# Performance work log

Hardware: AMD Instinct MI355X
Metric: run time of the kernel (lower is better)

The kernel has to match this reference:

```python
import jax, jax.numpy as jnp
import numpy as np

E, H, HD = 2048, 32, 64
SCALE = HD ** -0.5


def setup_inputs() -> dict:
    key = jax.random.key(0)
    ks = jax.random.split(key, 11)
    B, T, P = 16, 4, 4096
    S = P + T
    return {
        "hidden_states": jax.random.normal(ks[0], (B, T, E), jnp.float32),
        "past_key": jax.random.normal(ks[1], (1, H, P, HD), jnp.float32),
        "past_value": jax.random.normal(ks[2], (1, H, P, HD), jnp.float32),
        "attention_mask": jnp.zeros((B, 1, T, S), jnp.float32),
        "Wq": jax.random.normal(ks[3], (E, E), jnp.float32) * 0.02,
        "bq": jax.random.normal(ks[4], (E,), jnp.float32) * 0.02,
        "Wk": jax.random.normal(ks[5], (E, E), jnp.float32) * 0.02,
        "bk": jax.random.normal(ks[6], (E,), jnp.float32) * 0.02,
        "Wv": jax.random.normal(ks[7], (E, E), jnp.float32) * 0.02,
        "bv": jax.random.normal(ks[8], (E,), jnp.float32) * 0.02,
        "Wo": jax.random.normal(ks[9], (E, E), jnp.float32) * 0.02,
        "bo": jax.random.normal(ks[10], (E,), jnp.float32) * 0.02,
    }


def _shape(x, B, S):
    # [B,S,E] -> [B,H,S,hd]
    return x.reshape(B, S, H, HD).transpose(0, 2, 1, 3)


def reference(hidden_states, past_key, past_value, attention_mask,
              Wq, bq, Wk, bk, Wv, bv, Wo, bo):
    B, T, _ = hidden_states.shape
    # projections (torch Linear: x @ W.T + b); query pre-scaled
    q = _shape(hidden_states @ Wq.T + bq, B, T) * SCALE   # [B,H,T,hd]
    k_new = _shape(hidden_states @ Wk.T + bk, B, T)       # [B,H,T,hd]
    v_new = _shape(hidden_states @ Wv.T + bv, B, T)
    # cache stored with batch 1, broadcast (torch repeat) to B, then concat
    k_past = jnp.broadcast_to(past_key, (B,) + past_key.shape[1:])
    v_past = jnp.broadcast_to(past_value, (B,) + past_value.shape[1:])
    k = jnp.concatenate([k_past, k_new], axis=2)          # [B,H,S,hd]
    v = jnp.concatenate([v_past, v_new], axis=2)
    scores = jnp.einsum('bhtd,bhsd->bhts', q, k)          # [B,H,T,S]
    scores = scores + attention_mask                      # mask is [B,1,T,S]
    scores = jnp.maximum(scores, jnp.finfo(scores.dtype).min)
    w = jax.nn.softmax(scores, axis=-1)
    out = jnp.einsum('bhts,bhsd->bhtd', w, v)             # [B,H,T,hd]
    out = out.transpose(0, 2, 1, 3).reshape(B, T, E)
    return out @ Wo.T + bo
```

## Files before the change

### kernel.cpp

```cpp
#include <hip/hip_runtime.h>
#include <hip/hip_bf16.h>


typedef float f4 __attribute__((ext_vector_type(4)));
typedef short s8v __attribute__((ext_vector_type(8)));

#define NEG_HUGE (-3.402823466e38f)

__device__ inline unsigned short f2bs(float x) {
  union { float f; unsigned int u; } a; a.f = x;
  unsigned int u = a.u;
  u += 0x7fffu + ((u >> 16) & 1u);
  return (unsigned short)(u >> 16);
}
__device__ inline float bs2f(unsigned short s) {
  union { unsigned int u; float f; } a; a.u = ((unsigned int)s) << 16;
  return a.f;
}
__device__ inline unsigned int pk2(float a, float b) {
  union { __hip_bfloat162 v; unsigned int u; } c;
  c.v = __float22bfloat162_rn(make_float2(a, b));
  return c.u;
}
__device__ inline unsigned long long pack4(float a, float b, float c, float d) {
  return (unsigned long long)pk2(a, b) | ((unsigned long long)pk2(c, d) << 32);
}
__device__ inline s8v cvt8(f4 a, f4 b) {
  union { s8v s; unsigned int u[4]; } r;
  r.u[0] = pk2(a[0], a[1]); r.u[1] = pk2(a[2], a[3]);
  r.u[2] = pk2(b[0], b[1]); r.u[3] = pk2(b[2], b[3]);
  return r.s;
}
__device__ inline f4 mfma16(s8v a, s8v b, f4 c) {
  return __builtin_amdgcn_mfma_f32_16x16x32_bf16(a, b, c, 0, 0, 0);
}
__device__ inline f4 fzero() { f4 z = {0.f,0.f,0.f,0.f}; return z; }
__device__ inline float wave_sum(float v) {
  #pragma unroll
  for (int off = 32; off; off >>= 1) v += __shfl_xor(v, off, 64);
  return v;
}

__global__ __launch_bounds__(256) void k_qkv(
    const float* __restrict__ hs, const float* __restrict__ Wq,
    const float* __restrict__ Wk, const float* __restrict__ Wv,
    float* __restrict__ part) {
  __shared__ __align__(16) unsigned short As[64 * 264];
  const int n0 = blockIdx.x * 64;
  const int k0 = blockIdx.y * 256;
  const int p = n0 >> 11;
  const int c0 = n0 & 2047;
  const float* W = (p == 0) ? Wq : (p == 1) ? Wk : Wv;
  const int t = threadIdx.x, lane = t & 63, w = t >> 6;
  const int cl = lane & 15, quad = lane >> 4;

  #pragma unroll
  for (int i = 0; i < 16; ++i) {
    int idx4 = t + (i << 8);
    int row = idx4 >> 6;
    int col = (idx4 & 63) << 2;
    f4 v = *reinterpret_cast<const f4*>(hs + row * 2048 + k0 + col);
    *reinterpret_cast<unsigned long long*>(&As[row * 264 + col]) =
        pack4(v[0], v[1], v[2], v[3]);
  }
  __syncthreads();

  f4 acc[4];
  #pragma unroll
  for (int i = 0; i < 4; ++i) acc[i] = fzero();

  const int cw = c0 + w * 16 + cl;
  const float* wbase = W + (size_t)cw * 2048 + k0;
  #pragma unroll
  for (int ks2 = 0; ks2 < 8; ++ks2) {
    const int kb = ks2 * 32 + quad * 8;
    f4 w0 = *reinterpret_cast<const f4*>(wbase + kb);
    f4 w1 = *reinterpret_cast<const f4*>(wbase + kb + 4);
    s8v bf = cvt8(w0, w1);
    #pragma unroll
    for (int mt = 0; mt < 4; ++mt) {
      s8v af = *reinterpret_cast<const s8v*>(&As[(mt * 16 + cl) * 264 + kb]);
      acc[mt] = mfma16(af, bf, acc[mt]);
    }
  }
  float* outp = part + (size_t)blockIdx.y * 64 * 6144;
  #pragma unroll
  for (int mt = 0; mt < 4; ++mt)
    #pragma unroll
    for (int rg = 0; rg < 4; ++rg) {
      int r = mt * 16 + quad * 4 + rg;
      outp[r * 6144 + n0 + w * 16 + cl] = acc[mt][rg];
    }
}

__global__ __launch_bounds__(256) void k_qkv_red(
    const float* __restrict__ part, const float* __restrict__ bq,
    const float* __restrict__ bk, const float* __restrict__ bv,
    unsigned short* __restrict__ qws, float* __restrict__ knew,
    float* __restrict__ vnew) {
  const int i4 = blockIdx.x * 256 + threadIdx.x;
  const int base = i4 * 4;
  const int r = base / 6144;
  const int n = base - r * 6144;
  f4 s = *reinterpret_cast<const f4*>(part + base);
  #pragma unroll
  for (int ks = 1; ks < 8; ++ks) {
    f4 p2 = *reinterpret_cast<const f4*>(part + (size_t)ks * 393216 + base);
    #pragma unroll
    for (int j = 0; j < 4; ++j) s[j] += p2[j];
  }
  const int p = n >> 11, c = n & 2047;
  const int h = c >> 6, d = c & 63;
  const int b = r >> 2, tt = r & 3;
  if (p == 0) {
    f4 bb = *reinterpret_cast<const f4*>(bq + c);
    uint2 pw;
    pw.x = pk2((s[0] + bb[0]) * 0.125f, (s[1] + bb[1]) * 0.125f);
    pw.y = pk2((s[2] + bb[2]) * 0.125f, (s[3] + bb[3]) * 0.125f);
    *reinterpret_cast<uint2*>(qws + h * 4608 + r * 72 + d) = pw;
  } else if (p == 1) {
    f4 bb = *reinterpret_cast<const f4*>(bk + c);
    f4 o;
    #pragma unroll
    for (int j = 0; j < 4; ++j) o[j] = s[j] + bb[j];
    *reinterpret_cast<f4*>(knew + ((h * 16 + b) * 4 + tt) * 64 + d) = o;
  } else {
    f4 bb = *reinterpret_cast<const f4*>(bv + c);
    f4 o;
    #pragma unroll
    for (int j = 0; j < 4; ++j) o[j] = s[j] + bb[j];
    *reinterpret_cast<f4*>(vnew + ((h * 16 + b) * 4 + tt) * 64 + d) = o;
  }
}

__global__ __launch_bounds__(256) void k_flash(
    const unsigned short* __restrict__ qws, const float* __restrict__ Kp,
    const float* __restrict__ Vp, const float* __restrict__ mask,
    float* __restrict__ Opart, float* __restrict__ mpart,
    float* __restrict__ lpart) {
  __shared__ __align__(16) unsigned short Pl[64 * 264];
  __shared__ float redm[4 * 64];
  __shared__ float reds[4 * 64];
  const int bx = blockIdx.x;
  const int h = bx & 31, cch = bx >> 5;
  const int s0 = cch * 256;
  const int t = threadIdx.x, lane = t & 63, w = t >> 6;
  const int cl = lane & 15, quad = lane >> 4;
  const float* Kh = Kp + (size_t)h * 4096 * 64;
  const float* Vh = Vp + (size_t)h * 4096 * 64;

  s8v qf[4][2];
  #pragma unroll
  for (int qt = 0; qt < 4; ++qt)
    #pragma unroll
    for (int k2 = 0; k2 < 2; ++k2)
      qf[qt][k2] = *reinterpret_cast<const s8v*>(
          qws + h * 4608 + (qt * 16 + cl) * 72 + k2 * 32 + quad * 8);

  f4 acc[4][4];
  #pragma unroll
  for (int si = 0; si < 4; ++si)
    #pragma unroll
    for (int qt = 0; qt < 4; ++qt) acc[si][qt] = fzero();

  #pragma unroll
  for (int si = 0; si < 4; ++si) {
    const float* kr = Kh + (size_t)(s0 + w * 64 + si * 16 + cl) * 64 + quad * 8;
    #pragma unroll
    for (int k2 = 0; k2 < 2; ++k2) {
      f4 k0v = *reinterpret_cast<const f4*>(kr + k2 * 32);
      f4 k1v = *reinterpret_cast<const f4*>(kr + k2 * 32 + 4);
      s8v ak = cvt8(k0v, k1v);
      #pragma unroll
      for (int qt = 0; qt < 4; ++qt)
        acc[si][qt] = mfma16(ak, qf[qt][k2], acc[si][qt]);
    }
  }

  #pragma unroll
  for (int si = 0; si < 4; ++si)
    #pragma unroll
    for (int qt = 0; qt < 4; ++qt) {
      f4 mv = *reinterpret_cast<const f4*>(
          mask + (size_t)(qt * 16 + cl) * 4100 + s0 + w * 64 + si * 16 + quad * 4);
      #pragma unroll
      for (int rg = 0; rg < 4; ++rg)
        acc[si][qt][rg] = fmaxf(acc[si][qt][rg] + mv[rg], NEG_HUGE);
    }

  #pragma unroll
  for (int qt = 0; qt < 4; ++qt) {
    float m = NEG_HUGE;
    #pragma unroll
    for (int si = 0; si < 4; ++si)
      #pragma unroll
      for (int rg = 0; rg < 4; ++rg) m = fmaxf(m, acc[si][qt][rg]);
    m = fmaxf(m, __shfl_xor(m, 16, 64));
    m = fmaxf(m, __shfl_xor(m, 32, 64));
    if (quad == 0) redm[w * 64 + qt * 16 + cl] = m;
  }
  __syncthreads();

  float mq[4];
  #pragma unroll
  for (int qt = 0; qt < 4; ++qt) {
    int q = qt * 16 + cl;
    mq[qt] = fmaxf(fmaxf(redm[q], redm[64 + q]),
                   fmaxf(redm[128 + q], redm[192 + q]));
    if (w == 0 && quad == 0) mpart[(h * 16 + cch) * 64 + q] = mq[qt];
  }
  #pragma unroll
  for (int qt = 0; qt < 4; ++qt) {
    float sum = 0.f;
    #pragma unroll
    for (int si = 0; si < 4; ++si) {
      f4 e;
      #pragma unroll
      for (int rg = 0; rg < 4; ++rg) {
        e[rg] = __expf(acc[si][qt][rg] - mq[qt]);
        sum += e[rg];
      }
      uint2 pw;
      pw.x = pk2(e[0], e[1]);
      pw.y = pk2(e[2], e[3]);
      *reinterpret_cast<uint2*>(
          &Pl[(qt * 16 + cl) * 264 + w * 64 + si * 16 + quad * 4]) = pw;
    }
    sum += __shfl_xor(sum, 16, 64);
    sum += __shfl_xor(sum, 32, 64);
    if (quad == 0) reds[w * 64 + qt * 16 + cl] = sum;
  }
  __syncthreads();

  if (w == 0 && quad == 0) {
    #pragma unroll
    for (int qt = 0; qt < 4; ++qt) {
      int q = qt * 16 + cl;
      lpart[(h * 16 + cch) * 64 + q] =
          reds[q] + reds[64 + q] + reds[128 + q] + reds[192 + q];
    }
  }

  f4 oacc[4];
  #pragma unroll
  for (int mt = 0; mt < 4; ++mt) oacc[mt] = fzero();
  const int dcol = w * 16 + cl;
  #pragma unroll
  for (int k2 = 0; k2 < 8; ++k2) {
    const int sb = k2 * 32 + quad * 8;
    const float* vb = Vh + (size_t)(s0 + sb) * 64 + dcol;
    f4 v0, v1;
    v0[0] = vb[0];   v0[1] = vb[64];  v0[2] = vb[128]; v0[3] = vb[192];
    v1[0] = vb[256]; v1[1] = vb[320]; v1[2] = vb[384]; v1[3] = vb[448];
    s8v bvv = cvt8(v0, v1);
    #pragma unroll
    for (int mt = 0; mt < 4; ++mt) {
      s8v pa = *reinterpret_cast<const s8v*>(&Pl[(mt * 16 + cl) * 264 + sb]);
      oacc[mt] = mfma16(pa, bvv, oacc[mt]);
    }
  }
  float* ob = Opart + (size_t)(h * 16 + cch) * 64 * 64;
  #pragma unroll
  for (int mt = 0; mt < 4; ++mt)
    #pragma unroll
    for (int rg = 0; rg < 4; ++rg)
      ob[(mt * 16 + quad * 4 + rg) * 64 + dcol] = oacc[mt][rg];
}

__global__ __launch_bounds__(256) void k_merge(
    const unsigned short* __restrict__ qws, const float* __restrict__ knew,
    const float* __restrict__ vnew, const float* __restrict__ mask,
    const float* __restrict__ Opart, const float* __restrict__ mpart,
    const float* __restrict__ lpart, unsigned short* __restrict__ attn) {
  const int bx = blockIdx.x;
  const int h = bx & 31, b = bx >> 5;
  const int tt = threadIdx.x >> 6;
  const int d = threadIdx.x & 63;
  const int r = b * 4 + tt;
  float qd = bs2f(qws[h * 4608 + r * 72 + d]);
  float scn[4];
  #pragma unroll
  for (int tp = 0; tp < 4; ++tp) {
    float kn = knew[((h * 16 + b) * 4 + tp) * 64 + d];
    float s = wave_sum(qd * kn);
    s += mask[(size_t)r * 4100 + 4096 + tp];
    scn[tp] = fmaxf(s, NEG_HUGE);
  }
  float mi[16], li[16];
  float mtot = NEG_HUGE;
  #pragma unroll
  for (int i = 0; i < 16; ++i) {
    mi[i] = mpart[(h * 16 + i) * 64 + r];
    li[i] = lpart[(h * 16 + i) * 64 + r];
    mtot = fmaxf(mtot, mi[i]);
  }
  #pragma unroll
  for (int tp = 0; tp < 4; ++tp) mtot = fmaxf(mtot, scn[tp]);
  float ltot = 0.f, od = 0.f;
  #pragma unroll
  for (int i = 0; i < 16; ++i) {
    float fct = __expf(mi[i] - mtot);
    ltot += li[i] * fct;
    od += Opart[((size_t)(h * 16 + i) * 64 + r) * 64 + d] * fct;
  }
  #pragma unroll
  for (int tp = 0; tp < 4; ++tp) {
    float e = __expf(scn[tp] - mtot);
    ltot += e;
    od += e * vnew[((h * 16 + b) * 4 + tp) * 64 + d];
  }
  attn[(size_t)r * 2048 + h * 64 + d] = f2bs(od / ltot);
}

__global__ __launch_bounds__(256) void k_out(
    const unsigned short* __restrict__ attn, const float* __restrict__ Wo,
    float* __restrict__ part) {
  __shared__ __align__(16) unsigned short As[64 * 264];
  const int n0 = blockIdx.x * 64;
  const int ksb = blockIdx.y;
  const int k0 = ksb * 256;
  const int t = threadIdx.x, lane = t & 63, w = t >> 6;
  const int cl = lane & 15, quad = lane >> 4;
  #pragma unroll
  for (int i = 0; i < 8; ++i) {
    int idx8 = t + (i << 8);
    int row = idx8 >> 5;
    int col = (idx8 & 31) << 3;
    *reinterpret_cast<uint4*>(&As[row * 264 + col]) =
        *reinterpret_cast<const uint4*>(attn + (size_t)row * 2048 + k0 + col);
  }
  __syncthreads();
  f4 acc[4];
  #pragma unroll
  for (int i = 0; i < 4; ++i) acc[i] = fzero();
  const int cw = n0 + w * 16 + cl;
  const float* wbase = Wo + (size_t)cw * 2048 + k0;
  #pragma unroll
  for (int ks2 = 0; ks2 < 8; ++ks2) {
    const int kb = ks2 * 32 + quad * 8;
    f4 w0 = *reinterpret_cast<const f4*>(wbase + kb);
    f4 w1 = *reinterpret_cast<const f4*>(wbase + kb + 4);
    s8v bf = cvt8(w0, w1);
    #pragma unroll
    for (int mt = 0; mt < 4; ++mt) {
      s8v af = *reinterpret_cast<const s8v*>(&As[(mt * 16 + cl) * 264 + kb]);
      acc[mt] = mfma16(af, bf, acc[mt]);
    }
  }
  float* op = part + (size_t)ksb * 131072;
  #pragma unroll
  for (int mt = 0; mt < 4; ++mt)
    #pragma unroll
    for (int rg = 0; rg < 4; ++rg) {
      int r = mt * 16 + quad * 4 + rg;
      op[r * 2048 + n0 + w * 16 + cl] = acc[mt][rg];
    }
}

__global__ __launch_bounds__(256) void k_out_red(
    const float* __restrict__ part, const float* __restrict__ bo,
    float* __restrict__ out) {
  const int i4 = blockIdx.x * 256 + threadIdx.x;
  f4 s = *reinterpret_cast<const f4*>(part + (size_t)i4 * 4);
  #pragma unroll
  for (int ks = 1; ks < 8; ++ks) {
    f4 p2 = *reinterpret_cast<const f4*>(part + (size_t)ks * 131072 + (size_t)i4 * 4);
    #pragma unroll
    for (int j = 0; j < 4; ++j) s[j] += p2[j];
  }
  f4 bias = *reinterpret_cast<const f4*>(bo + (i4 & 511) * 4);
  f4 o;
  #pragma unroll
  for (int j = 0; j < 4; ++j) o[j] = s[j] + bias[j];
  *reinterpret_cast<f4*>(out + (size_t)i4 * 4) = o;
}

extern "C" void kernel_launch(void* const* d_in, const int* in_sizes, int n_in,
                              void* d_out, int out_size, void* d_ws, size_t ws_size,
                              hipStream_t stream) {
  const float* hs   = (const float*)d_in[0];
  const float* pk   = (const float*)d_in[1];
  const float* pv   = (const float*)d_in[2];
  const float* mask = (const float*)d_in[3];
  const float* Wq   = (const float*)d_in[4];
  const float* bq   = (const float*)d_in[5];
  const float* Wk   = (const float*)d_in[6];
  const float* bk   = (const float*)d_in[7];
  const float* Wv   = (const float*)d_in[8];
  const float* bv   = (const float*)d_in[9];
  const float* Wo   = (const float*)d_in[10];
  const float* bo   = (const float*)d_in[11];

  float* f = (float*)d_ws;
  float* qkv_part = f;
  float* o_part   = qkv_part + 3145728;
  float* Opart    = o_part   + 1048576;
  float* mpart    = Opart    + 2097152;
  float* lpart    = mpart    + 32768;
  float* knew     = lpart    + 32768;
  float* vnew     = knew     + 131072;
  unsigned short* qws  = (unsigned short*)(vnew + 131072);
  unsigned short* attn = qws + 147456;

  k_qkv<<<dim3(96, 8), 256, 0, stream>>>(hs, Wq, Wk, Wv, qkv_part);
  k_qkv_red<<<384, 256, 0, stream>>>(qkv_part, bq, bk, bv, qws, knew, vnew);
  k_flash<<<512, 256, 0, stream>>>(qws, pk, pv, mask, Opart, mpart, lpart);
  k_merge<<<512, 256, 0, stream>>>(qws, knew, vnew, mask, Opart, mpart, lpart, attn);
  k_out<<<dim3(32, 8), 256, 0, stream>>>(attn, Wo, o_part);
  k_out_red<<<128, 256, 0, stream>>>(o_part, bo, (float*)d_out);
}
```

Before: 196.6 us.

## Pre-convert activations to bf16 and read GEMM A operands directly from global

Adds a small prep kernel that converts hidden_states to bf16 once, so the QKV GEMM blocks read bf16 A fragments straight from global memory instead of each converting and staging them in LDS behind a barrier. The output projection also drops its LDS staging and doubles its K-split, using 16 partial slabs instead of 8 and summing more partials in the reduction. The aim is to cut redundant conversion work, LDS traffic and sync latency, and to add parallelism to the weight-bandwidth-bound out-projection. In exchange it adds a kernel launch, a larger partial buffer and extra reduction reads.

```diff
diff --git a/kernel.cpp b/kernel.cpp
--- a/kernel.cpp
+++ b/kernel.cpp
@@ -41,11 +41,24 @@
   return v;
 }
 
+__global__ __launch_bounds__(256) void k_prep(
+    const float* __restrict__ hs, unsigned short* __restrict__ hsb) {
+  const int idx = blockIdx.x * 256 + threadIdx.x;
+  const int base = idx * 8;
+  f4 a = *reinterpret_cast<const f4*>(hs + base);
+  f4 b = *reinterpret_cast<const f4*>(hs + base + 4);
+  unsigned long long p0 = pack4(a[0], a[1], a[2], a[3]);
+  unsigned long long p1 = pack4(b[0], b[1], b[2], b[3]);
+  uint4 o;
+  o.x = (unsigned int)p0; o.y = (unsigned int)(p0 >> 32);
+  o.z = (unsigned int)p1; o.w = (unsigned int)(p1 >> 32);
+  *reinterpret_cast<uint4*>(hsb + base) = o;
+}
+
 __global__ __launch_bounds__(256) void k_qkv(
-    const float* __restrict__ hs, const float* __restrict__ Wq,
+    const unsigned short* __restrict__ hsb, const float* __restrict__ Wq,
     const float* __restrict__ Wk, const float* __restrict__ Wv,
     float* __restrict__ part) {
-  __shared__ __align__(16) unsigned short As[64 * 264];
   const int n0 = blockIdx.x * 64;
   const int k0 = blockIdx.y * 256;
   const int p = n0 >> 11;
@@ -54,23 +67,13 @@
   const int t = threadIdx.x, lane = t & 63, w = t >> 6;
   const int cl = lane & 15, quad = lane >> 4;
 
-  #pragma unroll
-  for (int i = 0; i < 16; ++i) {
-    int idx4 = t + (i << 8);
-    int row = idx4 >> 6;
-    int col = (idx4 & 63) << 2;
-    f4 v = *reinterpret_cast<const f4*>(hs + row * 2048 + k0 + col);
-    *reinterpret_cast<unsigned long long*>(&As[row * 264 + col]) =
-        pack4(v[0], v[1], v[2], v[3]);
-  }
-  __syncthreads();
-
   f4 acc[4];
   #pragma unroll
   for (int i = 0; i < 4; ++i) acc[i] = fzero();
 
   const int cw = c0 + w * 16 + cl;
   const float* wbase = W + (size_t)cw * 2048 + k0;
+  const unsigned short* abase = hsb + k0;
   #pragma unroll
   for (int ks2 = 0; ks2 < 8; ++ks2) {
     const int kb = ks2 * 32 + quad * 8;
@@ -79,7 +82,7 @@
     s8v bf = cvt8(w0, w1);
     #pragma unroll
     for (int mt = 0; mt < 4; ++mt) {
-      s8v af = *reinterpret_cast<const s8v*>(&As[(mt * 16 + cl) * 264 + kb]);
+      s8v af = *reinterpret_cast<const s8v*>(abase + (mt * 16 + cl) * 2048 + kb);
       acc[mt] = mfma16(af, bf, acc[mt]);
     }
   }
@@ -315,39 +318,29 @@
 __global__ __launch_bounds__(256) void k_out(
     const unsigned short* __restrict__ attn, const float* __restrict__ Wo,
     float* __restrict__ part) {
-  __shared__ __align__(16) unsigned short As[64 * 264];
   const int n0 = blockIdx.x * 64;
-  const int ksb = blockIdx.y;
-  const int k0 = ksb * 256;
+  const int k0 = blockIdx.y * 128;
   const int t = threadIdx.x, lane = t & 63, w = t >> 6;
   const int cl = lane & 15, quad = lane >> 4;
-  #pragma unroll
-  for (int i = 0; i < 8; ++i) {
-    int idx8 = t + (i << 8);
-    int row = idx8 >> 5;
-    int col = (idx8 & 31) << 3;
-    *reinterpret_cast<uint4*>(&As[row * 264 + col]) =
-        *reinterpret_cast<const uint4*>(attn + (size_t)row * 2048 + k0 + col);
-  }
-  __syncthreads();
   f4 acc[4];
   #pragma unroll
   for (int i = 0; i < 4; ++i) acc[i] = fzero();
   const int cw = n0 + w * 16 + cl;
   const float* wbase = Wo + (size_t)cw * 2048 + k0;
-  #pragma unroll
-  for (int ks2 = 0; ks2 < 8; ++ks2) {
+  const unsigned short* abase = attn + k0;
+  #pragma unroll
+  for (int ks2 = 0; ks2 < 4; ++ks2) {
     const int kb = ks2 * 32 + quad * 8;
     f4 w0 = *reinterpret_cast<const f4*>(wbase + kb);
     f4 w1 = *reinterpret_cast<const f4*>(wbase + kb + 4);
     s8v bf = cvt8(w0, w1);
     #pragma unroll
     for (int mt = 0; mt < 4; ++mt) {
-      s8v af = *reinterpret_cast<const s8v*>(&As[(mt * 16 + cl) * 264 + kb]);
+      s8v af = *reinterpret_cast<const s8v*>(abase + (size_t)(mt * 16 + cl) * 2048 + kb);
       acc[mt] = mfma16(af, bf, acc[mt]);
     }
   }
-  float* op = part + (size_t)ksb * 131072;
+  float* op = part + (size_t)blockIdx.y * 131072;
   #pragma unroll
   for (int mt = 0; mt < 4; ++mt)
     #pragma unroll
@@ -363,7 +356,7 @@
   const int i4 = blockIdx.x * 256 + threadIdx.x;
   f4 s = *reinterpret_cast<const f4*>(part + (size_t)i4 * 4);
   #pragma unroll
-  for (int ks = 1; ks < 8; ++ks) {
+  for (int ks = 1; ks < 16; ++ks) {
     f4 p2 = *reinterpret_cast<const f4*>(part + (size_t)ks * 131072 + (size_t)i4 * 4);
     #pragma unroll
     for (int j = 0; j < 4; ++j) s[j] += p2[j];
@@ -394,18 +387,20 @@
   float* f = (float*)d_ws;
   float* qkv_part = f;
   float* o_part   = qkv_part + 3145728;
-  float* Opart    = o_part   + 1048576;
+  float* Opart    = o_part   + 2097152;
   float* mpart    = Opart    + 2097152;
   float* lpart    = mpart    + 32768;
   float* knew     = lpart    + 32768;
   float* vnew     = knew     + 131072;
   unsigned short* qws  = (unsigned short*)(vnew + 131072);
   unsigned short* attn = qws + 147456;
-
-  k_qkv<<<dim3(96, 8), 256, 0, stream>>>(hs, Wq, Wk, Wv, qkv_part);
+  unsigned short* hsb  = attn + 131072;
+
+  k_prep<<<64, 256, 0, stream>>>(hs, hsb);
+  k_qkv<<<dim3(96, 8), 256, 0, stream>>>(hsb, Wq, Wk, Wv, qkv_part);
   k_qkv_red<<<384, 256, 0, stream>>>(qkv_part, bq, bk, bv, qws, knew, vnew);
   k_flash<<<512, 256, 0, stream>>>(qws, pk, pv, mask, Opart, mpart, lpart);
   k_merge<<<512, 256, 0, stream>>>(qws, knew, vnew, mask, Opart, mpart, lpart, attn);
-  k_out<<<dim3(32, 8), 256, 0, stream>>>(attn, Wo, o_part);
+  k_out<<<dim3(32, 16), 256, 0, stream>>>(attn, Wo, o_part);
   k_out_red<<<128, 256, 0, stream>>>(o_part, bo, (float*)d_out);
 }
```

Result: slower. 207.2 us (+5.4%).
